# Kernel optimization log

Hardware: AMD Instinct MI355X
Metric: run time of the kernel (lower is better)

The kernel has to match this reference:

```python
import jax, jax.numpy as jnp
import numpy as np

B, H, W, C = 64, 14, 14, 768
HID = 4 * C            # ConvNeXt MLP hidden
E, K, R = 8, 2, 16     # num_experts, top_k, lora rank
SCALING = 16.0 / 16.0  # alpha / r


def setup_inputs() -> dict:
    key = jax.random.key(0)
    ks = jax.random.split(key, 9)
    N = B * H * W
    x = jax.random.normal(ks[0], (B, H, W, C), jnp.float32)
    p = jax.random.uniform(ks[1], (N, K), jnp.float32)
    topk_probs = p / (p.sum(-1, keepdims=True) + 1e-6)
    topk_idx = jax.random.randint(ks[2], (N, K), 0, E)
    w1 = jax.random.normal(ks[3], (C, HID), jnp.float32) * (C ** -0.5)
    b1 = jnp.zeros((HID,), jnp.float32)
    w2 = jax.random.normal(ks[4], (HID, C), jnp.float32) * (HID ** -0.5)
    b2 = jnp.zeros((C,), jnp.float32)
    w_down = jax.random.normal(ks[5], (E, C, R), jnp.float32) * (C ** -0.5)
    # torch init is zeros; use small randn so the op is numerically non-trivial
    w_up = jax.random.normal(ks[6], (E, R, C), jnp.float32) * 0.02
    return {"x": x, "topk_probs": topk_probs, "topk_idx": topk_idx,
            "w1": w1, "b1": b1, "w2": w2, "b2": b2,
            "w_down": w_down, "w_up": w_up}


def reference(x, topk_probs, topk_idx, w1, b1, w2, b2, w_down, w_up):
    # orig ConvNeXt MLP: Linear -> GELU(exact) -> Linear, pointwise over [B,H,W,C]
    h = jax.nn.gelu(jnp.einsum('bhwc,cf->bhwf', x, w1) + b1, approximate=False)
    orig = jnp.einsum('bhwf,fc->bhwc', h, w2) + b2

    N = x.shape[0] * x.shape[1] * x.shape[2]
    xf = x.reshape(N, C)  # [N, C] tokens
    # per-token combine weight for each expert: sum_k p[n,k] * 1[idx[n,k]==e]
    wt = (jax.nn.one_hot(topk_idx, E, dtype=xf.dtype) * topk_probs[..., None]).sum(1)  # [N, E]
    # dense-over-experts LoRA (vectorized form of the per-expert gather/scatter loop)
    down = jax.nn.gelu(jnp.einsum('nc,ecr->ner', xf, w_down), approximate=False)  # [N, E, R]
    up = jnp.einsum('ner,erc->nec', down, w_up) * SCALING                          # [N, E, C]
    moe = jnp.einsum('nec,ne->nc', up, wt)                                         # [N, C]
    return orig + moe.reshape(x.shape)
```

## Files before the change

kernel.cpp:

```cpp
#include <hip/hip_runtime.h>
#include <hip/hip_bf16.h>
#include <math.h>


#define NTOK   12544
#define CDIM   768
#define HIDDIM 3072
#define KBIG   3200

typedef __attribute__((ext_vector_type(8))) short bf16x8;
typedef __attribute__((ext_vector_type(4))) float f32x4;

#define GLOBAL_AS(p) ((const __attribute__((address_space(1))) void*)(p))
#define LDS_AS(p)    ((__attribute__((address_space(3))) void*)(p))
#define GLD(src, dst) __builtin_amdgcn_global_load_lds(GLOBAL_AS(src), LDS_AS(dst), 16, 0, 0)

__device__ inline unsigned short f2bf(float f) {
    unsigned int x = __float_as_uint(f);
    x += 0x7fffu + ((x >> 16) & 1u);
    return (unsigned short)(x >> 16);
}

__device__ inline float gelu_fast(float x) {
    float x3 = x * x * x;
    float u2 = 1.5957691216057308f * x + 0.07135481627260025f * x3;
    float e = __expf(-u2);
    return x * __builtin_amdgcn_rcpf(1.0f + e);
}

__global__ void __launch_bounds__(256) prep_kernel(
        const float* __restrict__ x, const float* __restrict__ w1,
        const float* __restrict__ w2, const float* __restrict__ wup,
        const float* __restrict__ wdn,
        unsigned short* __restrict__ xb, unsigned short* __restrict__ w1t,
        unsigned short* __restrict__ B2t, unsigned short* __restrict__ wdt) {
    __shared__ float tile[64][65];
    const int b = blockIdx.x, tid = threadIdx.x;
    if (b < 9408) {
        int i = b * 256 + tid;
        float4 v = ((const float4*)x)[i];
        ushort4 o;
        o.x = f2bf(v.x); o.y = f2bf(v.y); o.z = f2bf(v.z); o.w = f2bf(v.w);
        ((ushort4*)xb)[i] = o;
        return;
    }
    if (b < 10584) {
        const float* in; unsigned short* outp; int Ccols, out_ld, out_off, bx, by;
        if (b < 9984)       { int t = b - 9408;  in = w1;  outp = w1t; Ccols = 3072; out_ld = 768;  out_off = 0;    bx = t % 48; by = t / 48; }
        else if (b < 10560) { int t = b - 9984;  in = w2;  outp = B2t; Ccols = 768;  out_ld = 3200; out_off = 0;    bx = t % 12; by = t / 12; }
        else                { int t = b - 10560; in = wup; outp = B2t; Ccols = 768;  out_ld = 3200; out_off = 3072; bx = t % 12; by = t / 12; }
        const int c0 = bx * 64, r0 = by * 64;
        #pragma unroll
        for (int p = 0; p < 4; ++p) {
            int idx = p * 256 + tid;
            int r = idx >> 4, c4 = (idx & 15) * 4;
            float4 v = *(const float4*)&in[(size_t)(r0 + r) * Ccols + c0 + c4];
            tile[r][c4 + 0] = v.x; tile[r][c4 + 1] = v.y;
            tile[r][c4 + 2] = v.z; tile[r][c4 + 3] = v.w;
        }
        __syncthreads();
        #pragma unroll
        for (int p = 0; p < 2; ++p) {
            int u = p * 256 + tid;
            int cc = u >> 3, r8 = (u & 7) * 8;
            uint4 pk;
            pk.x = (unsigned)f2bf(tile[r8 + 0][cc]) | ((unsigned)f2bf(tile[r8 + 1][cc]) << 16);
            pk.y = (unsigned)f2bf(tile[r8 + 2][cc]) | ((unsigned)f2bf(tile[r8 + 3][cc]) << 16);
            pk.z = (unsigned)f2bf(tile[r8 + 4][cc]) | ((unsigned)f2bf(tile[r8 + 5][cc]) << 16);
            pk.w = (unsigned)f2bf(tile[r8 + 6][cc]) | ((unsigned)f2bf(tile[r8 + 7][cc]) << 16);
            *(uint4*)&outp[(size_t)(c0 + cc) * out_ld + out_off + r0 + r8] = pk;
        }
        return;
    }
    {
        int idx = (b - 10584) * 256 + tid;
        int j = idx / 768, c = idx - j * 768;
        int e = j >> 4, r = j & 15;
        wdt[idx] = f2bf(wdn[((size_t)e * 768 + c) * 16 + r]);
    }
}

template <int NFRAG, int P, bool TAILV, int VMN, class Issue>
__device__ __forceinline__ void phase4n(
        const char* lds, int aO0, int aO1, int bO0, int bO1,
        f32x4 (&acc)[4][NFRAG], bf16x8 (&bfr)[NFRAG][2], Issue issue) {
    bf16x8 af[2][2];
    #pragma unroll
    for (int f = 0; f < 2; ++f) {
        af[f][0] = *(const bf16x8*)(lds + aO0 + (2 * P + f) * 2048);
        af[f][1] = *(const bf16x8*)(lds + aO1 + (2 * P + f) * 2048);
    }
    if (P == 0) {
        #pragma unroll
        for (int nf = 0; nf < NFRAG; ++nf) {
            bfr[nf][0] = *(const bf16x8*)(lds + bO0 + nf * 2048);
            bfr[nf][1] = *(const bf16x8*)(lds + bO1 + nf * 2048);
        }
    }
    issue();
    __builtin_amdgcn_s_barrier();
    asm volatile("s_waitcnt lgkmcnt(0)" ::: "memory");
    __builtin_amdgcn_sched_barrier(0);
    __builtin_amdgcn_s_setprio(1);
    #pragma unroll
    for (int f = 0; f < 2; ++f)
        #pragma unroll
        for (int nf = 0; nf < NFRAG; ++nf)
            #pragma unroll
            for (int k = 0; k < 2; ++k)
                acc[2 * P + f][nf] = __builtin_amdgcn_mfma_f32_16x16x32_bf16(
                    af[f][k], bfr[nf][k], acc[2 * P + f][nf], 0, 0, 0);
    __builtin_amdgcn_s_setprio(0);
    if (TAILV) {
        if constexpr (VMN == 3) asm volatile("s_waitcnt vmcnt(3)" ::: "memory");
        else                    asm volatile("s_waitcnt vmcnt(2)" ::: "memory");
    }
    __builtin_amdgcn_s_barrier();
    __builtin_amdgcn_sched_barrier(0);
}

template <int EPI, int NBX, bool LORA>
__global__ void __launch_bounds__(512, 4)
gemm4_kernel(const unsigned short* __restrict__ A, int lda,
             const unsigned short* __restrict__ Bt, int ldb,
             int kTiles, const float* __restrict__ bias,
             unsigned short* __restrict__ apOut, float* __restrict__ fOut,
             const int* __restrict__ tki, const float* __restrict__ tkp,
             const unsigned short* __restrict__ Bt2) {
    __shared__ __align__(1024) char ldsraw[81920];
    char* ldsA = ldsraw;
    char* ldsB = ldsraw + 32768;

    constexpr int MAIN = NBX * (NTOK / 128);
    const int orig = blockIdx.x;

    const int tid  = threadIdx.x;
    const int wave = tid >> 6;
    const int lane = tid & 63;
    const int row16 = lane & 15;
    const int quad  = lane >> 4;
    const int wm = (wave >> 2) << 6;
    const int swz = (row16 & 7) << 4;
    const int aFB = ((wm + row16) << 7) + (quad << 4);
    const int aX0 = (aFB ^ swz), aX1 = ((aFB + 64) ^ swz);

    const int d  = tid << 4;
    const int s  = d ^ (((d >> 7) & 7) << 4);
    const int sr = s >> 7;
    const int sc = (s & 127) >> 1;
    const int ldsW = wave << 10;

    if constexpr (LORA) {
        if (orig >= MAIN) {
            const int m0 = (orig - MAIN) * 128;
            const int wn = (wave & 3) << 5;
            const int bFB = ((wn + row16) << 7) + (quad << 4);
            const int bX0 = (bFB ^ swz) + 32768, bX1 = ((bFB + 64) ^ swz) + 32768;
            const char* aSrc = (const char*)(A + (size_t)(m0 + sr) * lda + sc);
            const char* bSrc = (const char*)(Bt2 + (size_t)sr * CDIM + sc);
            const size_t aStep = (size_t)64 * lda * 2;
            const size_t bStep = (size_t)64 * CDIM * 2;
            auto issueA = [&](int b, int tk) {
                const char* sp = aSrc + (size_t)tk * 128;
                char* dp = ldsA + b * 16384 + ldsW;
                GLD(sp, dp);
                GLD(sp + aStep, dp + 8192);
            };
            auto issueB = [&](int b, int tk) {
                const char* sp = bSrc + (size_t)tk * 128;
                char* dp = ldsB + b * 16384 + ldsW;
                GLD(sp, dp);
                GLD(sp + bStep, dp + 8192);
            };
            f32x4 acc[4][2] = {};
            issueB(0, 0); issueA(0, 0); issueB(1, 1);
            asm volatile("s_waitcnt vmcnt(2)" ::: "memory");
            __builtin_amdgcn_s_barrier();
            __builtin_amdgcn_sched_barrier(0);
            const int nIter = kTiles >> 1;
            for (int it = 0; it < nIter; ++it) {
                const int t  = it * 2;
                const int t2 = (t + 2 < kTiles) ? t + 2 : 0;
                const int t3 = (t + 3 < kTiles) ? t + 3 : 0;
                bf16x8 bfr[2][2];
                phase4n<2, 0, false, 2>(ldsraw, aX0, aX1, bX0, bX1, acc, bfr,
                                        [&]{ issueA(1, t + 1); });
                phase4n<2, 1, true , 2>(ldsraw, aX0, aX1, bX0, bX1, acc, bfr,
                                        [&]{ issueB(0, t2); });
                phase4n<2, 0, false, 2>(ldsraw, aX0 + 16384, aX1 + 16384, bX0 + 16384, bX1 + 16384,
                                        acc, bfr, [&]{ issueA(0, t2); });
                phase4n<2, 1, true , 2>(ldsraw, aX0 + 16384, aX1 + 16384, bX0 + 16384, bX1 + 16384,
                                        acc, bfr, [&]{ issueB(1, t3); });
            }
            asm volatile("s_waitcnt vmcnt(0)" ::: "memory");
            #pragma unroll
            for (int mi = 0; mi < 4; ++mi) {
                #pragma unroll
                for (int i = 0; i < 4; ++i) {
                    const int m = m0 + wm + mi * 16 + quad * 4 + i;
                    const int i0 = tki[m * 2], i1 = tki[m * 2 + 1];
                    const float p0 = tkp[m * 2], p1 = tkp[m * 2 + 1];
                    #pragma unroll
                    for (int nf = 0; nf < 2; ++nf) {
                        const int col = wn + nf * 16 + row16;
                        const int e = col >> 4;
                        float wt = (i0 == e ? p0 : 0.f) + (i1 == e ? p1 : 0.f);
                        apOut[(size_t)m * KBIG + 3072 + col] =
                            f2bf(gelu_fast(acc[mi][nf][i]) * wt);
                    }
                }
            }
            return;
        }
    }

    constexpr int qq = MAIN / 8;
    const int xcd = orig & 7, within = orig >> 3;
    const int wgid = xcd * qq + within;
    const int bx = wgid % NBX, by = wgid / NBX;

    const int m0 = by * 128;
    const int n0 = bx * 192;
    const int wn = (wave & 3) * 48;
    const int bFB = ((wn + row16) << 7) + (quad << 4);
    const int bX0 = (bFB ^ swz) + 32768, bX1 = ((bFB + 64) ^ swz) + 32768;

    const char* aSrc = (const char*)(A + (size_t)(m0 + sr) * lda + sc);
    const char* bSrc = (const char*)(Bt + (size_t)(n0 + sr) * ldb + sc);
    const size_t aStep = (size_t)64 * lda * 2;
    const size_t bStep = (size_t)64 * ldb * 2;

    auto issueA = [&](int b, int tk) {
        const char* sp = aSrc + (size_t)tk * 128;
        char* dp = ldsA + b * 16384 + ldsW;
        GLD(sp, dp);
        GLD(sp + aStep, dp + 8192);
    };
    auto issueB = [&](int b, int tk) {
        const char* sp = bSrc + (size_t)tk * 128;
        char* dp = ldsB + b * 24576 + ldsW;
        GLD(sp, dp);
        GLD(sp + bStep, dp + 8192);
        GLD(sp + 2 * bStep, dp + 16384);
    };

    f32x4 acc[4][3] = {};

    issueB(0, 0);
    issueA(0, 0);
    issueB(1, 1);
    asm volatile("s_waitcnt vmcnt(3)" ::: "memory");
    __builtin_amdgcn_s_barrier();
    __builtin_amdgcn_sched_barrier(0);

    const int nIter = kTiles >> 1;
    for (int it = 0; it < nIter; ++it) {
        const int t  = it * 2;
        const int t2 = (t + 2 < kTiles) ? t + 2 : 0;
        const int t3 = (t + 3 < kTiles) ? t + 3 : 0;
        bf16x8 bfr[3][2];
        phase4n<3, 0, false, 3>(ldsraw, aX0, aX1, bX0, bX1, acc, bfr,
                                [&]{ issueA(1, t + 1); });
        phase4n<3, 1, true , 3>(ldsraw, aX0, aX1, bX0, bX1, acc, bfr,
                                [&]{ issueB(0, t2); });
        phase4n<3, 0, false, 3>(ldsraw, aX0 + 16384, aX1 + 16384, bX0 + 24576, bX1 + 24576,
                                acc, bfr, [&]{ issueA(0, t2); });
        phase4n<3, 1, true , 3>(ldsraw, aX0 + 16384, aX1 + 16384, bX0 + 24576, bX1 + 24576,
                                acc, bfr, [&]{ issueB(1, t3); });
    }
    asm volatile("s_waitcnt vmcnt(0)" ::: "memory");

    float bv[3];
    #pragma unroll
    for (int nf = 0; nf < 3; ++nf) bv[nf] = bias[n0 + wn + nf * 16 + row16];
    #pragma unroll
    for (int mi = 0; mi < 4; ++mi) {
        #pragma unroll
        for (int i = 0; i < 4; ++i) {
            const int m = m0 + wm + mi * 16 + quad * 4 + i;
            #pragma unroll
            for (int nf = 0; nf < 3; ++nf) {
                const int col = n0 + wn + nf * 16 + row16;
                float v = acc[mi][nf][i] + bv[nf];
                if (EPI == 0) apOut[(size_t)m * KBIG + col] = f2bf(gelu_fast(v));
                else          fOut[(size_t)m * CDIM + col] = v;
            }
        }
    }
}


extern "C" void kernel_launch(void* const* d_in, const int* in_sizes, int n_in,
                              void* d_out, int out_size, void* d_ws, size_t ws_size,
                              hipStream_t stream) {
    const float* x   = (const float*)d_in[0];
    const float* tkp = (const float*)d_in[1];
    const int*   tki = (const int*)d_in[2];
    const float* w1  = (const float*)d_in[3];
    const float* b1  = (const float*)d_in[4];
    const float* w2  = (const float*)d_in[5];
    const float* b2  = (const float*)d_in[6];
    const float* wdn = (const float*)d_in[7];
    const float* wup = (const float*)d_in[8];
    float* out = (float*)d_out;

    unsigned short* xb  = (unsigned short*)d_ws;
    unsigned short* w1t = xb  + (size_t)NTOK * CDIM;
    unsigned short* B2t = w1t + (size_t)HIDDIM * CDIM;
    unsigned short* wdt = B2t + (size_t)CDIM * KBIG;
    unsigned short* Ap  = wdt + (size_t)128 * CDIM;

    prep_kernel<<<dim3(10968), 256, 0, stream>>>(x, w1, w2, wup, wdn,
                                                 xb, w1t, B2t, wdt);

    gemm4_kernel<0, HIDDIM / 192, true>
        <<<dim3((HIDDIM / 192 + 1) * (NTOK / 128)), 512, 0, stream>>>(
        xb, CDIM, w1t, CDIM, CDIM / 64, b1, Ap, nullptr, tki, tkp, wdt);
    gemm4_kernel<2, CDIM / 192, false>
        <<<dim3((CDIM / 192) * (NTOK / 128)), 512, 0, stream>>>(
        Ap, KBIG, B2t, KBIG, KBIG / 64, b2, nullptr, out, nullptr, nullptr, nullptr);
}
```

Baseline: 252.5 us.

## Swap MFMA operands for row-contiguous epilogue stores and hoist LDS fragment loads

The MFMA operand order is swapped so each lane's four accumulators hold four consecutive output columns of one row rather than four rows of one column. This lets the epilogue write ushort4 and float4 vector stores and load the bias as a float4, replacing scattered scalar stores. The A and B fragment LDS reads for both phases of a k-tile pair are also hoisted ahead of the two phases. That raises register pressure under the 512x4 launch bounds, and the LDS reads are now less interleaved with the MFMA work.

```diff
diff --git a/kernel.cpp b/kernel.cpp
--- a/kernel.cpp
+++ b/kernel.cpp
@@ -81,22 +81,9 @@
 }
 
 template <int NFRAG, int P, bool TAILV, int VMN, class Issue>
-__device__ __forceinline__ void phase4n(
-        const char* lds, int aO0, int aO1, int bO0, int bO1,
-        f32x4 (&acc)[4][NFRAG], bf16x8 (&bfr)[NFRAG][2], Issue issue) {
-    bf16x8 af[2][2];
-    #pragma unroll
-    for (int f = 0; f < 2; ++f) {
-        af[f][0] = *(const bf16x8*)(lds + aO0 + (2 * P + f) * 2048);
-        af[f][1] = *(const bf16x8*)(lds + aO1 + (2 * P + f) * 2048);
-    }
-    if (P == 0) {
-        #pragma unroll
-        for (int nf = 0; nf < NFRAG; ++nf) {
-            bfr[nf][0] = *(const bf16x8*)(lds + bO0 + nf * 2048);
-            bfr[nf][1] = *(const bf16x8*)(lds + bO1 + nf * 2048);
-        }
-    }
+__device__ __forceinline__ void phase4s(
+        f32x4 (&acc)[4][NFRAG], const bf16x8 (&af)[4][2],
+        const bf16x8 (&bfr)[NFRAG][2], Issue issue) {
     issue();
     __builtin_amdgcn_s_barrier();
     asm volatile("s_waitcnt lgkmcnt(0)" ::: "memory");
@@ -109,7 +96,7 @@
             #pragma unroll
             for (int k = 0; k < 2; ++k)
                 acc[2 * P + f][nf] = __builtin_amdgcn_mfma_f32_16x16x32_bf16(
-                    af[f][k], bfr[nf][k], acc[2 * P + f][nf], 0, 0, 0);
+                    bfr[nf][k], af[2 * P + f][k], acc[2 * P + f][nf], 0, 0, 0);
     __builtin_amdgcn_s_setprio(0);
     if (TAILV) {
         if constexpr (VMN == 3) asm volatile("s_waitcnt vmcnt(3)" ::: "memory");
@@ -182,32 +169,49 @@
                 const int t  = it * 2;
                 const int t2 = (t + 2 < kTiles) ? t + 2 : 0;
                 const int t3 = (t + 3 < kTiles) ? t + 3 : 0;
-                bf16x8 bfr[2][2];
-                phase4n<2, 0, false, 2>(ldsraw, aX0, aX1, bX0, bX1, acc, bfr,
-                                        [&]{ issueA(1, t + 1); });
-                phase4n<2, 1, true , 2>(ldsraw, aX0, aX1, bX0, bX1, acc, bfr,
-                                        [&]{ issueB(0, t2); });
-                phase4n<2, 0, false, 2>(ldsraw, aX0 + 16384, aX1 + 16384, bX0 + 16384, bX1 + 16384,
-                                        acc, bfr, [&]{ issueA(0, t2); });
-                phase4n<2, 1, true , 2>(ldsraw, aX0 + 16384, aX1 + 16384, bX0 + 16384, bX1 + 16384,
-                                        acc, bfr, [&]{ issueB(1, t3); });
+                bf16x8 af[4][2], bfr[2][2];
+                #pragma unroll
+                for (int mi = 0; mi < 4; ++mi) {
+                    af[mi][0] = *(const bf16x8*)(ldsraw + aX0 + mi * 2048);
+                    af[mi][1] = *(const bf16x8*)(ldsraw + aX1 + mi * 2048);
+                }
+                #pragma unroll
+                for (int nf = 0; nf < 2; ++nf) {
+                    bfr[nf][0] = *(const bf16x8*)(ldsraw + bX0 + nf * 2048);
+                    bfr[nf][1] = *(const bf16x8*)(ldsraw + bX1 + nf * 2048);
+                }
+                phase4s<2, 0, false, 2>(acc, af, bfr, [&]{ issueA(1, t + 1); });
+                phase4s<2, 1, true , 2>(acc, af, bfr, [&]{ issueB(0, t2); });
+                #pragma unroll
+                for (int mi = 0; mi < 4; ++mi) {
+                    af[mi][0] = *(const bf16x8*)(ldsraw + aX0 + 16384 + mi * 2048);
+                    af[mi][1] = *(const bf16x8*)(ldsraw + aX1 + 16384 + mi * 2048);
+                }
+                #pragma unroll
+                for (int nf = 0; nf < 2; ++nf) {
+                    bfr[nf][0] = *(const bf16x8*)(ldsraw + bX0 + 16384 + nf * 2048);
+                    bfr[nf][1] = *(const bf16x8*)(ldsraw + bX1 + 16384 + nf * 2048);
+                }
+                phase4s<2, 0, false, 2>(acc, af, bfr, [&]{ issueA(0, t2); });
+                phase4s<2, 1, true , 2>(acc, af, bfr, [&]{ issueB(1, t3); });
             }
             asm volatile("s_waitcnt vmcnt(0)" ::: "memory");
             #pragma unroll
             for (int mi = 0; mi < 4; ++mi) {
-                #pragma unroll
-                for (int i = 0; i < 4; ++i) {
-                    const int m = m0 + wm + mi * 16 + quad * 4 + i;
-                    const int i0 = tki[m * 2], i1 = tki[m * 2 + 1];
-                    const float p0 = tkp[m * 2], p1 = tkp[m * 2 + 1];
-                    #pragma unroll
-                    for (int nf = 0; nf < 2; ++nf) {
-                        const int col = wn + nf * 16 + row16;
-                        const int e = col >> 4;
-                        float wt = (i0 == e ? p0 : 0.f) + (i1 == e ? p1 : 0.f);
-                        apOut[(size_t)m * KBIG + 3072 + col] =
-                            f2bf(gelu_fast(acc[mi][nf][i]) * wt);
-                    }
+                const int m = m0 + wm + mi * 16 + row16;
+                const int i0 = tki[m * 2], i1 = tki[m * 2 + 1];
+                const float p0 = tkp[m * 2], p1 = tkp[m * 2 + 1];
+                #pragma unroll
+                for (int nf = 0; nf < 2; ++nf) {
+                    const int nb = wn + nf * 16 + quad * 4;
+                    const int e = nb >> 4;
+                    const float wt = (i0 == e ? p0 : 0.f) + (i1 == e ? p1 : 0.f);
+                    ushort4 o;
+                    o.x = f2bf(gelu_fast(acc[mi][nf][0]) * wt);
+                    o.y = f2bf(gelu_fast(acc[mi][nf][1]) * wt);
+                    o.z = f2bf(gelu_fast(acc[mi][nf][2]) * wt);
+                    o.w = f2bf(gelu_fast(acc[mi][nf][3]) * wt);
+                    *(ushort4*)&apOut[(size_t)m * KBIG + 3072 + nb] = o;
                 }
             }
             return;
@@ -258,32 +262,58 @@
         const int t  = it * 2;
         const int t2 = (t + 2 < kTiles) ? t + 2 : 0;
         const int t3 = (t + 3 < kTiles) ? t + 3 : 0;
-        bf16x8 bfr[3][2];
-        phase4n<3, 0, false, 3>(ldsraw, aX0, aX1, bX0, bX1, acc, bfr,
-                                [&]{ issueA(1, t + 1); });
-        phase4n<3, 1, true , 3>(ldsraw, aX0, aX1, bX0, bX1, acc, bfr,
-                                [&]{ issueB(0, t2); });
-        phase4n<3, 0, false, 3>(ldsraw, aX0 + 16384, aX1 + 16384, bX0 + 24576, bX1 + 24576,
-                                acc, bfr, [&]{ issueA(0, t2); });
-        phase4n<3, 1, true , 3>(ldsraw, aX0 + 16384, aX1 + 16384, bX0 + 24576, bX1 + 24576,
-                                acc, bfr, [&]{ issueB(1, t3); });
+        bf16x8 af[4][2], bfr[3][2];
+        #pragma unroll
+        for (int mi = 0; mi < 4; ++mi) {
+            af[mi][0] = *(const bf16x8*)(ldsraw + aX0 + mi * 2048);
+            af[mi][1] = *(const bf16x8*)(ldsraw + aX1 + mi * 2048);
+        }
+        #pragma unroll
+        for (int nf = 0; nf < 3; ++nf) {
+            bfr[nf][0] = *(const bf16x8*)(ldsraw + bX0 + nf * 2048);
+            bfr[nf][1] = *(const bf16x8*)(ldsraw + bX1 + nf * 2048);
+        }
+        phase4s<3, 0, false, 3>(acc, af, bfr, [&]{ issueA(1, t + 1); });
+        phase4s<3, 1, true , 3>(acc, af, bfr, [&]{ issueB(0, t2); });
+        #pragma unroll
+        for (int mi = 0; mi < 4; ++mi) {
+            af[mi][0] = *(const bf16x8*)(ldsraw + aX0 + 16384 + mi * 2048);
+            af[mi][1] = *(const bf16x8*)(ldsraw + aX1 + 16384 + mi * 2048);
+        }
+        #pragma unroll
+        for (int nf = 0; nf < 3; ++nf) {
+            bfr[nf][0] = *(const bf16x8*)(ldsraw + bX0 + 24576 + nf * 2048);
+            bfr[nf][1] = *(const bf16x8*)(ldsraw + bX1 + 24576 + nf * 2048);
+        }
+        phase4s<3, 0, false, 3>(acc, af, bfr, [&]{ issueA(0, t2); });
+        phase4s<3, 1, true , 3>(acc, af, bfr, [&]{ issueB(1, t3); });
     }
     asm volatile("s_waitcnt vmcnt(0)" ::: "memory");
 
-    float bv[3];
+    float4 bv[3];
     #pragma unroll
-    for (int nf = 0; nf < 3; ++nf) bv[nf] = bias[n0 + wn + nf * 16 + row16];
+    for (int nf = 0; nf < 3; ++nf)
+        bv[nf] = *(const float4*)&bias[n0 + wn + nf * 16 + quad * 4];
     #pragma unroll
     for (int mi = 0; mi < 4; ++mi) {
-        #pragma unroll
-        for (int i = 0; i < 4; ++i) {
-            const int m = m0 + wm + mi * 16 + quad * 4 + i;
-            #pragma unroll
-            for (int nf = 0; nf < 3; ++nf) {
-                const int col = n0 + wn + nf * 16 + row16;
-                float v = acc[mi][nf][i] + bv[nf];
-                if (EPI == 0) apOut[(size_t)m * KBIG + col] = f2bf(gelu_fast(v));
-                else          fOut[(size_t)m * CDIM + col] = v;
+        const int m = m0 + wm + mi * 16 + row16;
+        #pragma unroll
+        for (int nf = 0; nf < 3; ++nf) {
+            const int nb = n0 + wn + nf * 16 + quad * 4;
+            if (EPI == 0) {
+                ushort4 o;
+                o.x = f2bf(gelu_fast(acc[mi][nf][0] + bv[nf].x));
+                o.y = f2bf(gelu_fast(acc[mi][nf][1] + bv[nf].y));
+                o.z = f2bf(gelu_fast(acc[mi][nf][2] + bv[nf].z));
+                o.w = f2bf(gelu_fast(acc[mi][nf][3] + bv[nf].w));
+                *(ushort4*)&apOut[(size_t)m * KBIG + nb] = o;
+            } else {
+                float4 v;
+                v.x = acc[mi][nf][0] + bv[nf].x;
+                v.y = acc[mi][nf][1] + bv[nf].y;
+                v.z = acc[mi][nf][2] + bv[nf].z;
+                v.w = acc[mi][nf][3] + bv[nf].w;
+                *(float4*)&fOut[(size_t)m * CDIM + nb] = v;
             }
         }
     }
```

New measurement: 278.2 us. 1.1x slower.
